# Kernel optimization log

Measured on AMD Instinct MI355X. Metric: run time of the kernel, lower is better.

Reference implementation:

```python
import jax, jax.numpy as jnp
import numpy as np

N_NODES = 100000
N_REL = 8
N_EDGES = 100000  # per relation
DIM = 128


def setup_inputs() -> dict:
    key = jax.random.key(0)
    ks = jax.random.split(key, 8)
    s = 1.0 / np.sqrt(DIM)
    return {
        "entity_embeddings": jax.random.normal(ks[0], (N_NODES, DIM), jnp.float32),
        "edge_index": jax.random.randint(ks[1], (N_REL, 2, N_EDGES), 0, N_NODES, jnp.int32),
        "edge_weights": jax.random.uniform(ks[2], (N_REL, N_EDGES), jnp.float32),
        "relW1": jax.random.normal(ks[3], (N_REL, DIM, DIM), jnp.float32) * s,
        "selfW1": jax.random.normal(ks[4], (DIM, DIM), jnp.float32) * s,
        "bias1": jnp.zeros((N_REL, DIM), jnp.float32),
        "relW2": jax.random.normal(ks[5], (N_REL, DIM, DIM), jnp.float32) * s,
        "selfW2": jax.random.normal(ks[6], (DIM, DIM), jnp.float32) * s,
        "bias2": jnp.zeros((N_REL, DIM), jnp.float32),
    }


def _wrgcn_layer(x, edge_index, edge_weights, relW, selfW, bias):
    # x: [N, Din]; edge_index: [R, 2, E]; edge_weights: [R, E]
    N = x.shape[0]
    R, _, E = edge_index.shape
    src = edge_index[:, 0]  # [R, E]
    tgt = edge_index[:, 1]  # [R, E]
    # gather -> per-relation matmul -> edge-weight scale
    src_emb = x[src]  # [R, E, Din]
    msg = jnp.einsum('red,rdo->reo', src_emb, relW) * edge_weights[..., None]  # [R, E, Dout]
    # scatter-add to target nodes (shared node space across relations)
    agg = jax.ops.segment_sum(msg.reshape(R * E, -1), tgt.reshape(R * E), num_segments=N)
    # bias added once per (relation, unique target node)
    tgt_mask = jnp.zeros((R, N), x.dtype).at[jnp.arange(R)[:, None], tgt].set(1.0)  # [R, N]
    agg = agg + jnp.einsum('rn,ro->no', tgt_mask, bias)
    # self loop
    return agg + x @ selfW


def reference(entity_embeddings, edge_index, edge_weights,
              relW1, selfW1, bias1, relW2, selfW2, bias2):
    h = _wrgcn_layer(entity_embeddings, edge_index, edge_weights, relW1, selfW1, bias1)
    h = jax.nn.relu(h)  # dropout is identity in eval mode
    out = _wrgcn_layer(h, edge_index, edge_weights, relW2, selfW2, bias2)
    return out
```

## Files before the change

kernel.cpp:

```cpp
#include <hip/hip_runtime.h>
#include <hip/hip_bf16.h>

#define NN 100000
#define DD 128
#define RR 8
#define EE 100000
#define NP1 (NN + 1)
#define NB1 98
#define PADN (NB1 * 1024)
#define SEG 8
#define WPR (NN / SEG)

typedef __attribute__((ext_vector_type(8))) short short8;
typedef __attribute__((ext_vector_type(4))) float f32x4;

__device__ __forceinline__ unsigned short f2bf(float v) {
  union { float f; unsigned int u; } x; x.f = v;
  unsigned int r = (x.u + 0x7FFFu + ((x.u >> 16) & 1u)) >> 16;
  return (unsigned short)r;
}

__global__ void k_cast4(const float* __restrict__ src, unsigned short* __restrict__ dst, int n4) {
  int i = blockIdx.x * blockDim.x + threadIdx.x;
  int stride = gridDim.x * blockDim.x;
  for (; i < n4; i += stride) {
    float4 v = reinterpret_cast<const float4*>(src)[i];
    ushort4 o;
    o.x = f2bf(v.x); o.y = f2bf(v.y); o.z = f2bf(v.z); o.w = f2bf(v.w);
    reinterpret_cast<ushort4*>(dst)[i] = o;
  }
}

__global__ void k_castT2(const float* __restrict__ s1, unsigned short* __restrict__ d1,
                         const float* __restrict__ s2, unsigned short* __restrict__ d2,
                         int total) {
  int i = blockIdx.x * blockDim.x + threadIdx.x;
  if (i >= total) return;
  const float* src = blockIdx.y ? s2 : s1;
  unsigned short* dst = blockIdx.y ? d2 : d1;
  int r = i >> 14;
  int k = (i >> 7) & 127;
  int o = i & 127;
  dst[(r << 14) + (o << 7) + k] = f2bf(src[i]);
}

__global__ void k_zero2(unsigned int* __restrict__ p1, int n1,
                        unsigned int* __restrict__ p2, int n2) {
  int i = blockIdx.x * blockDim.x + threadIdx.x;
  if (i < n1) p1[i] = 0u;
  else if (i - n1 < n2) p2[i - n1] = 0u;
}

__global__ void k_hist_mask(const int* __restrict__ edge_index, int* __restrict__ cnt,
                            unsigned int* __restrict__ mb) {
  int e = blockIdx.x * blockDim.x + threadIdx.x;
  int r = blockIdx.y;
  if (e >= EE) return;
  int tgt = edge_index[(size_t)r * 2 * EE + EE + e];
  atomicAdd(&cnt[r * PADN + tgt], 1);
  atomicOr(&mb[tgt], 1u << r);
}

__global__ void k_scan1(const int* __restrict__ cnt, int* __restrict__ start, int* __restrict__ bsum) {
  const int r = blockIdx.y, b = blockIdx.x, t = threadIdx.x;
  const int bin0 = b * 1024 + t * 4;
  int4 c = *reinterpret_cast<const int4*>(&cnt[r * PADN + bin0]);
  int s1 = c.x, s2 = s1 + c.y, s3 = s2 + c.z, tot = s3 + c.w;
  __shared__ int sh[256];
  sh[t] = tot;
  __syncthreads();
  for (int off = 1; off < 256; off <<= 1) {
    int v = (t >= off) ? sh[t - off] : 0;
    __syncthreads();
    sh[t] += v;
    __syncthreads();
  }
  int excl = sh[t] - tot;
  if (t == 255) bsum[r * NB1 + b] = sh[255];
  const int base = r * NP1;
  if (bin0 < NN) start[base + bin0] = excl;
  if (bin0 + 1 < NN) start[base + bin0 + 1] = excl + s1;
  if (bin0 + 2 < NN) start[base + bin0 + 2] = excl + s2;
  if (bin0 + 3 < NN) start[base + bin0 + 3] = excl + s3;
}

__global__ void k_scan2(const int* __restrict__ bsum, int* __restrict__ boff, int* __restrict__ start) {
  const int r = blockIdx.x, t = threadIdx.x;
  int v = (t < NB1) ? bsum[r * NB1 + t] : 0;
  __shared__ int sh[128];
  sh[t] = v;
  __syncthreads();
  for (int off = 1; off < 128; off <<= 1) {
    int u = (t >= off) ? sh[t - off] : 0;
    __syncthreads();
    sh[t] += u;
    __syncthreads();
  }
  if (t < NB1) boff[r * NB1 + t] = sh[t] - v;
  if (t == 0) start[r * NP1 + NN] = EE;
}

__global__ void k_scan3(int* __restrict__ start, const int* __restrict__ boff, int* __restrict__ cursor) {
  const int r = blockIdx.y, b = blockIdx.x, t = threadIdx.x;
  const int bin0 = b * 1024 + t * 4;
  const int off = boff[r * NB1 + b];
  const int base = r * NP1;
#pragma unroll
  for (int k = 0; k < 4; ++k) {
    int bin = bin0 + k;
    if (bin < NN) {
      int v = start[base + bin] + off;
      start[base + bin] = v;
      cursor[r * NN + bin] = v;
    }
  }
}

__global__ void k_scatter2(const int* __restrict__ edge_index, const float* __restrict__ ew,
                           int* __restrict__ cursor, int2* __restrict__ es) {
  int e = blockIdx.x * blockDim.x + threadIdx.x;
  int r = blockIdx.y;
  if (e >= EE) return;
  const int* src_p = edge_index + (size_t)r * 2 * EE;
  int tgt = src_p[EE + e];
  int pos = atomicAdd(&cursor[r * NN + tgt], 1);
  es[(size_t)r * EE + pos] = make_int2(src_p[e], __float_as_int(ew[(size_t)r * EE + e]));
}

__device__ __forceinline__ void preagg_wave(const unsigned short* __restrict__ Xsrc,
                                            const int2* __restrict__ es,
                                            const int* __restrict__ start,
                                            int r, int n0, int lane,
                                            float (&a0)[SEG], float (&a1)[SEG]) {
  const size_t rEE = (size_t)r * EE;
  int b = start[r * NP1 + n0 + (lane < 8 ? lane : 8)];
  int p[SEG + 1];
#pragma unroll
  for (int i = 0; i <= SEG; ++i) p[i] = __builtin_amdgcn_readlane(b, i);
#pragma unroll
  for (int i = 0; i < SEG; ++i) { a0[i] = 0.f; a1[i] = 0.f; }
  const int p0 = p[0];
  const int count = p[SEG] - p0;
  if (count <= 0) return;
  int rounds = 0;
#pragma unroll
  for (int i = 0; i < SEG; ++i) rounds = max(rounds, p[i + 1] - p[i]);
  const unsigned int* Xu = reinterpret_cast<const unsigned int*>(Xsrc);

  if (count <= 64) {
    int wl = lane < count ? lane : count - 1;
    int2 ew = es[rEE + p0 + wl];
    int esrc = ew.x;
    int ewbits = ew.y;
    for (int j = 0; j < rounds; ++j) {
#pragma unroll
      for (int i = 0; i < SEG; ++i) {
        int pos = p[i] + j;
        if (pos < p[i + 1]) {
          int widx = pos - p0;
          int s = __builtin_amdgcn_readlane(esrc, widx);
          float wv = __int_as_float(__builtin_amdgcn_readlane(ewbits, widx));
          unsigned int d = Xu[(size_t)s * 64 + lane];
          union { unsigned int u; float f; } lo, hi;
          lo.u = d << 16;
          hi.u = d & 0xFFFF0000u;
          a0[i] += wv * lo.f;
          a1[i] += wv * hi.f;
        }
      }
    }
  } else {
    for (int j = 0; j < rounds; ++j) {
#pragma unroll
      for (int i = 0; i < SEG; ++i) {
        int pos = p[i] + j;
        if (pos < p[i + 1]) {
          int2 e = es[rEE + pos];
          float wv = __int_as_float(e.y);
          unsigned int d = Xu[(size_t)e.x * 64 + lane];
          union { unsigned int u; float f; } lo, hi;
          lo.u = d << 16;
          hi.u = d & 0xFFFF0000u;
          a0[i] += wv * lo.f;
          a1[i] += wv * hi.f;
        }
      }
    }
  }
}

__launch_bounds__(256, 4)
__global__ void k_preagg_seg3(const unsigned short* __restrict__ Xsrc,
                              const int2* __restrict__ es, const int* __restrict__ start,
                              unsigned short* __restrict__ P0, unsigned short* __restrict__ P1,
                              unsigned short* __restrict__ P2,
                              int rbase, int nrel) {
  const int wid = blockIdx.x * 4 + (threadIdx.x >> 6);
  if (wid >= nrel * WPR) return;
  const int lane = threadIdx.x & 63;
  const int rr = wid / WPR;
  const int n0 = (wid - rr * WPR) * SEG;
  float a0[SEG], a1[SEG];
  preagg_wave(Xsrc, es, start, rbase + rr, n0, lane, a0, a1);
  unsigned short* P = (rr == 0) ? P0 : ((rr == 1) ? P1 : P2);
  unsigned int* Pw = reinterpret_cast<unsigned int*>(P);
#pragma unroll
  for (int i = 0; i < SEG; ++i)
    Pw[(size_t)(n0 + i) * 64 + lane] = (unsigned int)f2bf(a0[i]) | ((unsigned int)f2bf(a1[i]) << 16);
}

__launch_bounds__(256, 4)
__global__ void k_preagg_seg8(const unsigned short* __restrict__ Xsrc,
                              const int2* __restrict__ es, const int* __restrict__ start,
                              unsigned short* __restrict__ P0, unsigned short* __restrict__ Pws) {
  const int wid = blockIdx.x * 4 + (threadIdx.x >> 6);
  if (wid >= RR * WPR) return;
  const int lane = threadIdx.x & 63;
  const int rr = wid / WPR;
  const int n0 = (wid - rr * WPR) * SEG;
  float a0[SEG], a1[SEG];
  preagg_wave(Xsrc, es, start, rr, n0, lane, a0, a1);
  unsigned short* P = (rr == 0) ? P0 : (Pws + (size_t)(rr - 1) * NN * DD);
  unsigned int* Pw = reinterpret_cast<unsigned int*>(P);
#pragma unroll
  for (int i = 0; i < SEG; ++i)
    Pw[(size_t)(n0 + i) * 64 + lane] = (unsigned int)f2bf(a0[i]) | ((unsigned int)f2bf(a1[i]) << 16);
}

typedef const __attribute__((address_space(1))) void* gas1_t;
typedef __attribute__((address_space(3))) void* las3_t;

__device__ __forceinline__ void gl16(const void* g, void* s) {
  __builtin_amdgcn_global_load_lds((gas1_t)g, (las3_t)s, 16, 0, 0);
}

template <bool CLAMP>
__device__ __forceinline__ void stage_half(const unsigned short* __restrict__ g,
                                           unsigned short* lds, int t, int row0, int half) {
  const int w = t >> 6, l = t & 63;
  const int sub = l >> 3;
  const int sl = l & 7;
#pragma unroll
  for (int c = 0; c < 4; ++c) {
    int rb8 = c * 32 + w * 8;
    int row = rb8 + sub;
    int grow = row0 + row;
    int sr = CLAMP ? (grow < NN ? grow : NN - 1) : grow;
    const unsigned short* src = g + (size_t)sr * 128 + half * 64 + ((sl ^ (row & 7)) << 3);
    gl16(src, lds + rb8 * 64);
  }
}

__device__ __forceinline__ void mfma_half(const unsigned short* __restrict__ lA,
                                          const unsigned short* __restrict__ lB,
                                          f32x4 (&acc)[2][8], int w, int l) {
  const int lrow = l & 15, kgrp = l >> 4;
#pragma unroll
  for (int ks = 0; ks < 2; ++ks) {
    int kc = ks * 4 + kgrp;
    int ra = w * 32 + lrow;
    int rb = ra + 16;
    short8 a0 = *reinterpret_cast<const short8*>(&lA[(ra << 6) + ((kc ^ (ra & 7)) << 3)]);
    short8 a1 = *reinterpret_cast<const short8*>(&lA[(rb << 6) + ((kc ^ (rb & 7)) << 3)]);
#pragma unroll
    for (int ct = 0; ct < 8; ++ct) {
      int ro = ct * 16 + lrow;
      short8 b = *reinterpret_cast<const short8*>(&lB[(ro << 6) + ((kc ^ (ro & 7)) << 3)]);
      acc[0][ct] = __builtin_amdgcn_mfma_f32_16x16x32_bf16(a0, b, acc[0][ct], 0, 0, 0);
      acc[1][ct] = __builtin_amdgcn_mfma_f32_16x16x32_bf16(a1, b, acc[1][ct], 0, 0, 0);
    }
  }
}

template <bool CLAMP>
__device__ __forceinline__ void stage_lds(const unsigned short* __restrict__ g,
                                          unsigned short* lds, int t, int row0) {
  const int w = t >> 6, l = t & 63;
  const int sub = l >> 4, s = l & 15;
#pragma unroll
  for (int c = 0; c < 8; ++c) {
    int rowblk = c * 16 + w * 4;
    int row = rowblk + sub;
    int grow = row0 + row;
    int sr = CLAMP ? (grow < NN ? grow : NN - 1) : grow;
    const unsigned short* src = g + (size_t)sr * 128 + ((s ^ (row & 7)) << 3);
    gl16(src, lds + rowblk * 128);
  }
}

__device__ __forceinline__ void mfma_tile(const unsigned short* __restrict__ lA,
                                          const unsigned short* __restrict__ lB,
                                          f32x4 (&acc)[2][8], int w, int l) {
  const int lrow = l & 15, kgrp = l >> 4;
#pragma unroll
  for (int ks = 0; ks < 4; ++ks) {
    int kc = ks * 4 + kgrp;
    int ra = w * 32 + lrow;
    int rb = ra + 16;
    short8 a0 = *reinterpret_cast<const short8*>(&lA[(ra << 7) + ((kc ^ (ra & 7)) << 3)]);
    short8 a1 = *reinterpret_cast<const short8*>(&lA[(rb << 7) + ((kc ^ (rb & 7)) << 3)]);
#pragma unroll
    for (int ct = 0; ct < 8; ++ct) {
      int ro = ct * 16 + lrow;
      short8 b = *reinterpret_cast<const short8*>(&lB[(ro << 7) + ((kc ^ (ro & 7)) << 3)]);
      acc[0][ct] = __builtin_amdgcn_mfma_f32_16x16x32_bf16(a0, b, acc[0][ct], 0, 0, 0);
      acc[1][ct] = __builtin_amdgcn_mfma_f32_16x16x32_bf16(a1, b, acc[1][ct], 0, 0, 0);
    }
  }
}

template <bool L1>
__launch_bounds__(256, 2)
__global__ void k_gemm_fused(const unsigned short* __restrict__ Aself,
                             const unsigned short* __restrict__ Wself,
                             const unsigned short* __restrict__ P0,
                             const unsigned short* __restrict__ Pws,
                             const unsigned short* __restrict__ Wrel,
                             const unsigned int* __restrict__ maskbits,
                             const float* __restrict__ bias,
                             void* __restrict__ outp) {
  __shared__ __align__(16) unsigned short lA[2][128 * 64];
  __shared__ __align__(16) unsigned short lB[2][128 * 64];
  const int t = threadIdx.x;
  const int row0 = blockIdx.x * 128;
  const int w = t >> 6, l = t & 63;
  const int lrow = l & 15, kgrp = l >> 4;
  f32x4 acc[2][8] = {};

  auto A_of = [&](int term) -> const unsigned short* {
    return term == 0 ? Aself : (term == 1 ? P0 : Pws + (size_t)(term - 2) * NN * DD);
  };
  auto B_of = [&](int term) -> const unsigned short* {
    return term == 0 ? Wself : Wrel + ((term - 1) << 14);
  };

  stage_half<true>(A_of(0), lA[0], t, row0, 0);
  stage_half<false>(B_of(0), lB[0], t, 0, 0);
  __syncthreads();

  int cur = 0;
#pragma unroll 1
  for (int st = 0; st < 18; ++st) {
    if (st < 17) {
      int nt = (st + 1) >> 1, nh = (st + 1) & 1;
      stage_half<true>(A_of(nt), lA[cur ^ 1], t, row0, nh);
      stage_half<false>(B_of(nt), lB[cur ^ 1], t, 0, nh);
    }
    mfma_half(lA[cur], lB[cur], acc, w, l);
    __syncthreads();
    cur ^= 1;
  }

  {
    short8 a0 = {}, a1 = {}, bf[8];
#pragma unroll
    for (int ct = 0; ct < 8; ++ct) bf[ct] = short8{};
    if (kgrp == 0) {
      int ra = row0 + w * 32 + lrow;
      int rb = ra + 16;
      unsigned int ma = (ra < NN) ? maskbits[ra] : 0u;
      unsigned int mb = (rb < NN) ? maskbits[rb] : 0u;
#pragma unroll
      for (int k = 0; k < 8; ++k) {
        a0[k] = (short)(((ma >> k) & 1u) ? 0x3F80 : 0);
        a1[k] = (short)(((mb >> k) & 1u) ? 0x3F80 : 0);
      }
#pragma unroll
      for (int ct = 0; ct < 8; ++ct) {
        int o = ct * 16 + lrow;
#pragma unroll
        for (int k = 0; k < 8; ++k) bf[ct][k] = (short)f2bf(bias[k * 128 + o]);
      }
    }
#pragma unroll
    for (int ct = 0; ct < 8; ++ct) {
      acc[0][ct] = __builtin_amdgcn_mfma_f32_16x16x32_bf16(a0, bf[ct], acc[0][ct], 0, 0, 0);
      acc[1][ct] = __builtin_amdgcn_mfma_f32_16x16x32_bf16(a1, bf[ct], acc[1][ct], 0, 0, 0);
    }
  }

#pragma unroll
  for (int rt = 0; rt < 2; ++rt) {
#pragma unroll
    for (int j = 0; j < 4; ++j) {
      int grow = row0 + w * 32 + rt * 16 + kgrp * 4 + j;
      if (grow < NN) {
        if (L1) {
          unsigned short* op = (unsigned short*)outp + (size_t)grow * 128 + lrow;
#pragma unroll
          for (int ct = 0; ct < 8; ++ct) op[ct * 16] = f2bf(fmaxf(acc[rt][ct][j], 0.f));
        } else {
          float* op = (float*)outp + (size_t)grow * 128 + lrow;
#pragma unroll
          for (int ct = 0; ct < 8; ++ct) op[ct * 16] = acc[rt][ct][j];
        }
      }
    }
  }
}

template <int NT>
__launch_bounds__(256, 2)
__global__ void k_gemm_multi(const unsigned short* __restrict__ A0, const unsigned short* __restrict__ W0,
                             const unsigned short* __restrict__ A1, const unsigned short* __restrict__ W1,
                             const unsigned short* __restrict__ A2, const unsigned short* __restrict__ W2,
                             const unsigned short* __restrict__ A3, const unsigned short* __restrict__ W3,
                             float* __restrict__ outp, int accum) {
  __shared__ __align__(16) unsigned short lA[128 * 128];
  __shared__ __align__(16) unsigned short lB[128 * 128];
  const int t = threadIdx.x;
  const int row0 = blockIdx.x * 128;
  const int w = t >> 6, l = t & 63;
  const int lrow = l & 15, kgrp = l >> 4;
  f32x4 acc[2][8] = {};

  const unsigned short* As[4] = {A0, A1, A2, A3};
  const unsigned short* Ws[4] = {W0, W1, W2, W3};
#pragma unroll
  for (int term = 0; term < NT; ++term) {
    if (term) __syncthreads();
    stage_lds<true>(As[term], lA, t, row0);
    stage_lds<false>(Ws[term], lB, t, 0);
    __syncthreads();
    mfma_tile(lA, lB, acc, w, l);
  }

#pragma unroll
  for (int rt = 0; rt < 2; ++rt) {
#pragma unroll
    for (int j = 0; j < 4; ++j) {
      int grow = row0 + w * 32 + rt * 16 + kgrp * 4 + j;
      if (grow < NN) {
        float* op = outp + (size_t)grow * 128 + lrow;
        if (accum) {
#pragma unroll
          for (int ct = 0; ct < 8; ++ct) op[ct * 16] += acc[rt][ct][j];
        } else {
#pragma unroll
          for (int ct = 0; ct < 8; ++ct) op[ct * 16] = acc[rt][ct][j];
        }
      }
    }
  }
}

__global__ void k_epi1(const float* __restrict__ h32, const unsigned int* __restrict__ maskbits,
                       const float* __restrict__ bias, unsigned short* __restrict__ hb) {
  int gid = blockIdx.x * blockDim.x + threadIdx.x;
  if (gid >= NN * 32) return;
  int n = gid >> 5, c = (gid & 31) << 2;
  float4 v = *reinterpret_cast<const float4*>(h32 + (size_t)n * 128 + c);
  unsigned int mb = maskbits[n];
  float b0 = 0, b1 = 0, b2 = 0, b3 = 0;
#pragma unroll
  for (int r = 0; r < RR; ++r) {
    if ((mb >> r) & 1u) {
      const float* bp = bias + r * 128 + c;
      b0 += bp[0]; b1 += bp[1]; b2 += bp[2]; b3 += bp[3];
    }
  }
  ushort4 o;
  o.x = f2bf(fmaxf(v.x + b0, 0.f));
  o.y = f2bf(fmaxf(v.y + b1, 0.f));
  o.z = f2bf(fmaxf(v.z + b2, 0.f));
  o.w = f2bf(fmaxf(v.w + b3, 0.f));
  *reinterpret_cast<ushort4*>(hb + (size_t)n * 128 + c) = o;
}

__global__ void k_epi2(float* __restrict__ out, const unsigned int* __restrict__ maskbits,
                       const float* __restrict__ bias) {
  int gid = blockIdx.x * blockDim.x + threadIdx.x;
  if (gid >= NN * 32) return;
  int n = gid >> 5, c = (gid & 31) << 2;
  unsigned int mb = maskbits[n];
  if (!mb) return;
  float b0 = 0, b1 = 0, b2 = 0, b3 = 0;
#pragma unroll
  for (int r = 0; r < RR; ++r) {
    if ((mb >> r) & 1u) {
      const float* bp = bias + r * 128 + c;
      b0 += bp[0]; b1 += bp[1]; b2 += bp[2]; b3 += bp[3];
    }
  }
  float* p = out + (size_t)n * 128 + c;
  float4 v = *reinterpret_cast<const float4*>(p);
  v.x += b0; v.y += b1; v.z += b2; v.w += b3;
  *reinterpret_cast<float4*>(p) = v;
}

extern "C" void kernel_launch(void* const* d_in, const int* in_sizes, int n_in,
                              void* d_out, int out_size, void* d_ws, size_t ws_size,
                              hipStream_t stream) {
  const float* X   = (const float*)d_in[0];
  const int*   EI  = (const int*)d_in[1];
  const float* EW  = (const float*)d_in[2];
  const float* rW1 = (const float*)d_in[3];
  const float* sW1 = (const float*)d_in[4];
  const float* b1  = (const float*)d_in[5];
  const float* rW2 = (const float*)d_in[6];
  const float* sW2 = (const float*)d_in[7];
  const float* b2  = (const float*)d_in[8];
  float* out = (float*)d_out;
  char* ws = (char*)d_ws;

  size_t off = 0;
  auto take = [&](size_t sz) { char* p = ws + off; off += (sz + 255) & ~(size_t)255; return p; };
  unsigned short* Xb   = (unsigned short*)take((size_t)NN * DD * 2);
  unsigned short* hb   = (unsigned short*)take((size_t)NN * DD * 2);
  unsigned int*  maskb = (unsigned int*)take((size_t)NN * 4);
  unsigned short* rW1t = (unsigned short*)take((size_t)RR * DD * DD * 2);
  unsigned short* sW1t = (unsigned short*)take((size_t)DD * DD * 2);
  unsigned short* rW2t = (unsigned short*)take((size_t)RR * DD * DD * 2);
  unsigned short* sW2t = (unsigned short*)take((size_t)DD * DD * 2);
  int*   cnt    = (int*)take((size_t)RR * PADN * 4);
  int*   start  = (int*)take((size_t)RR * NP1 * 4);
  int*   cursor = (int*)take((size_t)RR * NN * 4);
  int*   bsum   = (int*)take((size_t)RR * NB1 * 4);
  int*   boff   = (int*)take((size_t)RR * NB1 * 4);
  int2*  es     = (int2*)take((size_t)RR * EE * 8);

  const size_t szReg = ((size_t)NN * DD * 2 + 255) & ~(size_t)255;
  const bool bigA = (off + 7 * szReg <= ws_size);
  unsigned short* Pws = nullptr;
  float* h32 = nullptr;
  if (bigA) {
    Pws = (unsigned short*)take(7 * szReg);
  } else {
    h32 = (float*)take((size_t)NN * DD * 4);
  }

  k_cast4<<<2048, 256, 0, stream>>>(X, Xb, NN * DD / 4);
  k_castT2<<<dim3((RR * DD * DD + 255) / 256, 2), 256, 0, stream>>>(rW1, rW1t, rW2, rW2t, RR * DD * DD);
  k_castT2<<<dim3((DD * DD + 255) / 256, 2), 256, 0, stream>>>(sW1, sW1t, sW2, sW2t, DD * DD);

  k_zero2<<<(NN + RR * PADN + 255) / 256, 256, 0, stream>>>(maskb, NN, (unsigned int*)cnt, RR * PADN);
  k_hist_mask<<<dim3((EE + 255) / 256, RR), 256, 0, stream>>>(EI, cnt, maskb);
  k_scan1<<<dim3(NB1, RR), 256, 0, stream>>>(cnt, start, bsum);
  k_scan2<<<RR, 128, 0, stream>>>(bsum, boff, start);
  k_scan3<<<dim3(NB1, RR), 256, 0, stream>>>(start, boff, cursor);
  k_scatter2<<<dim3((EE + 255) / 256, RR), 256, 0, stream>>>(EI, EW, cursor, es);

  const int nblk = (NN + 127) / 128;
  unsigned short* outu = (unsigned short*)d_out;

  if (bigA) {
    const int pblk = (RR * WPR + 3) / 4;
    k_preagg_seg8<<<pblk, 256, 0, stream>>>(Xb, es, start, outu, Pws);
    k_gemm_fused<true><<<nblk, 256, 0, stream>>>(Xb, sW1t, outu, Pws, rW1t, maskb, b1, hb);
    k_preagg_seg8<<<pblk, 256, 0, stream>>>(hb, es, start, Xb, Pws);
    k_gemm_fused<false><<<nblk, 256, 0, stream>>>(hb, sW2t, Xb, Pws, rW2t, maskb, b2, out);
  } else {
    unsigned short* h32u = (unsigned short*)h32;
    const int pblk3 = (3 * WPR + 3) / 4;
    const int pblk2 = (2 * WPR + 3) / 4;
    {
      unsigned short* P0 = outu;
      unsigned short* P1 = outu + (size_t)NN * DD;
      unsigned short* P2 = hb;
      k_preagg_seg3<<<pblk3, 256, 0, stream>>>(Xb, es, start, P0, P1, P2, 0, 3);
      k_gemm_multi<4><<<nblk, 256, 0, stream>>>(Xb, sW1t, P0, rW1t, P1, rW1t + (1 << 14), P2, rW1t + (2 << 14), h32, 0);
      k_preagg_seg3<<<pblk3, 256, 0, stream>>>(Xb, es, start, P0, P1, P2, 3, 3);
      k_gemm_multi<3><<<nblk, 256, 0, stream>>>(P0, rW1t + (3 << 14), P1, rW1t + (4 << 14), P2, rW1t + (5 << 14), nullptr, nullptr, h32, 1);
      k_preagg_seg3<<<pblk2, 256, 0, stream>>>(Xb, es, start, P0, P1, P2, 6, 2);
      k_gemm_multi<2><<<nblk, 256, 0, stream>>>(P0, rW1t + (6 << 14), P1, rW1t + (7 << 14), nullptr, nullptr, nullptr, nullptr, h32, 1);
    }
    k_epi1<<<(NN * 32 + 255) / 256, 256, 0, stream>>>(h32, maskb, b1, hb);
    {
      unsigned short* P0 = h32u;
      unsigned short* P1 = h32u + (size_t)NN * DD;
      unsigned short* P2 = Xb;
      k_preagg_seg3<<<pblk3, 256, 0, stream>>>(hb, es, start, P0, P1, P2, 0, 3);
      k_gemm_multi<4><<<nblk, 256, 0, stream>>>(hb, sW2t, P0, rW2t, P1, rW2t + (1 << 14), P2, rW2t + (2 << 14), out, 0);
      k_preagg_seg3<<<pblk3, 256, 0, stream>>>(hb, es, start, P0, P1, P2, 3, 3);
      k_gemm_multi<3><<<nblk, 256, 0, stream>>>(P0, rW2t + (3 << 14), P1, rW2t + (4 << 14), P2, rW2t + (5 << 14), nullptr, nullptr, out, 1);
      k_preagg_seg3<<<pblk2, 256, 0, stream>>>(hb, es, start, P0, P1, P2, 6, 2);
      k_gemm_multi<2><<<nblk, 256, 0, stream>>>(P0, rW2t + (6 << 14), P1, rW2t + (7 << 14), nullptr, nullptr, nullptr, nullptr, out, 1);
    }
    k_epi2<<<(NN * 32 + 255) / 256, 256, 0, stream>>>(out, maskb, b2);
  }
}
```

Baseline: 426.9 us.

## Merge prep kernels, widen preagg segments, single-buffer GEMM LDS for occupancy

Merges the weight transpose-cast and zeroing kernels into a single prep launch. Doubles the number of nodes each preagg wave handles (SEG 8 to 16) and raises the launch-bounds occupancy hints on the preagg and GEMM kernels. Turns the fused GEMM's double-buffered LDS staging into a single buffer with an extra barrier, halving shared memory so more blocks can be resident. This gives up load/compute overlap in the GEMM and may raise register pressure in preagg, since SEG 16 doubles the accumulator arrays under a tighter register cap.

```diff
diff --git a/kernel.cpp b/kernel.cpp
--- a/kernel.cpp
+++ b/kernel.cpp
@@ -8,7 +8,7 @@
 #define NP1 (NN + 1)
 #define NB1 98
 #define PADN (NB1 * 1024)
-#define SEG 8
+#define SEG 16
 #define WPR (NN / SEG)
 
 typedef __attribute__((ext_vector_type(8))) short short8;
@@ -31,25 +31,43 @@
   }
 }
 
-__global__ void k_castT2(const float* __restrict__ s1, unsigned short* __restrict__ d1,
-                         const float* __restrict__ s2, unsigned short* __restrict__ d2,
-                         int total) {
-  int i = blockIdx.x * blockDim.x + threadIdx.x;
-  if (i >= total) return;
-  const float* src = blockIdx.y ? s2 : s1;
-  unsigned short* dst = blockIdx.y ? d2 : d1;
-  int r = i >> 14;
-  int k = (i >> 7) & 127;
-  int o = i & 127;
-  dst[(r << 14) + (o << 7) + k] = f2bf(src[i]);
-}
-
-__global__ void k_zero2(unsigned int* __restrict__ p1, int n1,
-                        unsigned int* __restrict__ p2, int n2) {
-  int i = blockIdx.x * blockDim.x + threadIdx.x;
-  if (i < n1) p1[i] = 0u;
-  else if (i - n1 < n2) p2[i - n1] = 0u;
-}
+#define NWR (RR * DD * DD)
+#define NWS (DD * DD)
+__global__ void k_prep_small(const float* __restrict__ rW1, unsigned short* __restrict__ rW1t,
+                             const float* __restrict__ sW1, unsigned short* __restrict__ sW1t,
+                             const float* __restrict__ rW2, unsigned short* __restrict__ rW2t,
+                             const float* __restrict__ sW2, unsigned short* __restrict__ sW2t,
+                             unsigned int* __restrict__ maskb, unsigned int* __restrict__ cnt) {
+  int j = blockIdx.x * blockDim.x + threadIdx.x;
+  if (j < NWR) {
+    int r = j >> 14, k = (j >> 7) & 127, o = j & 127;
+    rW1t[(r << 14) + (o << 7) + k] = f2bf(rW1[j]);
+    return;
+  }
+  j -= NWR;
+  if (j < NWR) {
+    int r = j >> 14, k = (j >> 7) & 127, o = j & 127;
+    rW2t[(r << 14) + (o << 7) + k] = f2bf(rW2[j]);
+    return;
+  }
+  j -= NWR;
+  if (j < NWS) {
+    int k = j >> 7, o = j & 127;
+    sW1t[(o << 7) + k] = f2bf(sW1[j]);
+    return;
+  }
+  j -= NWS;
+  if (j < NWS) {
+    int k = j >> 7, o = j & 127;
+    sW2t[(o << 7) + k] = f2bf(sW2[j]);
+    return;
+  }
+  j -= NWS;
+  if (j < NN) { maskb[j] = 0u; return; }
+  j -= NN;
+  if (j < RR * PADN) cnt[j] = 0u;
+}
+#define PREP_TOTAL (2 * NWR + 2 * NWS + NN + RR * PADN)
 
 __global__ void k_hist_mask(const int* __restrict__ edge_index, int* __restrict__ cnt,
                             unsigned int* __restrict__ mb) {
@@ -133,7 +151,7 @@
                                             int r, int n0, int lane,
                                             float (&a0)[SEG], float (&a1)[SEG]) {
   const size_t rEE = (size_t)r * EE;
-  int b = start[r * NP1 + n0 + (lane < 8 ? lane : 8)];
+  int b = start[r * NP1 + n0 + (lane < SEG ? lane : SEG)];
   int p[SEG + 1];
 #pragma unroll
   for (int i = 0; i <= SEG; ++i) p[i] = __builtin_amdgcn_readlane(b, i);
@@ -189,7 +207,7 @@
   }
 }
 
-__launch_bounds__(256, 4)
+__launch_bounds__(256, 8)
 __global__ void k_preagg_seg3(const unsigned short* __restrict__ Xsrc,
                               const int2* __restrict__ es, const int* __restrict__ start,
                               unsigned short* __restrict__ P0, unsigned short* __restrict__ P1,
@@ -209,7 +227,7 @@
     Pw[(size_t)(n0 + i) * 64 + lane] = (unsigned int)f2bf(a0[i]) | ((unsigned int)f2bf(a1[i]) << 16);
 }
 
-__launch_bounds__(256, 4)
+__launch_bounds__(256, 8)
 __global__ void k_preagg_seg8(const unsigned short* __restrict__ Xsrc,
                               const int2* __restrict__ es, const int* __restrict__ start,
                               unsigned short* __restrict__ P0, unsigned short* __restrict__ Pws) {
@@ -310,7 +328,7 @@
 }
 
 template <bool L1>
-__launch_bounds__(256, 2)
+__launch_bounds__(256, 4)
 __global__ void k_gemm_fused(const unsigned short* __restrict__ Aself,
                              const unsigned short* __restrict__ Wself,
                              const unsigned short* __restrict__ P0,
@@ -319,8 +337,8 @@
                              const unsigned int* __restrict__ maskbits,
                              const float* __restrict__ bias,
                              void* __restrict__ outp) {
-  __shared__ __align__(16) unsigned short lA[2][128 * 64];
-  __shared__ __align__(16) unsigned short lB[2][128 * 64];
+  __shared__ __align__(16) unsigned short lA[128 * 64];
+  __shared__ __align__(16) unsigned short lB[128 * 64];
   const int t = threadIdx.x;
   const int row0 = blockIdx.x * 128;
   const int w = t >> 6, l = t & 63;
@@ -334,21 +352,14 @@
     return term == 0 ? Wself : Wrel + ((term - 1) << 14);
   };
 
-  stage_half<true>(A_of(0), lA[0], t, row0, 0);
-  stage_half<false>(B_of(0), lB[0], t, 0, 0);
-  __syncthreads();
-
-  int cur = 0;
 #pragma unroll 1
   for (int st = 0; st < 18; ++st) {
-    if (st < 17) {
-      int nt = (st + 1) >> 1, nh = (st + 1) & 1;
-      stage_half<true>(A_of(nt), lA[cur ^ 1], t, row0, nh);
-      stage_half<false>(B_of(nt), lB[cur ^ 1], t, 0, nh);
-    }
-    mfma_half(lA[cur], lB[cur], acc, w, l);
+    int nt = st >> 1, nh = st & 1;
+    stage_half<true>(A_of(nt), lA, t, row0, nh);
+    stage_half<false>(B_of(nt), lB, t, 0, nh);
     __syncthreads();
-    cur ^= 1;
+    mfma_half(lA, lB, acc, w, l);
+    if (st < 17) __syncthreads();
   }
 
   {
@@ -530,10 +541,10 @@
   }
 
   k_cast4<<<2048, 256, 0, stream>>>(X, Xb, NN * DD / 4);
-  k_castT2<<<dim3((RR * DD * DD + 255) / 256, 2), 256, 0, stream>>>(rW1, rW1t, rW2, rW2t, RR * DD * DD);
-  k_castT2<<<dim3((DD * DD + 255) / 256, 2), 256, 0, stream>>>(sW1, sW1t, sW2, sW2t, DD * DD);
-
-  k_zero2<<<(NN + RR * PADN + 255) / 256, 256, 0, stream>>>(maskb, NN, (unsigned int*)cnt, RR * PADN);
+  k_prep_small<<<(PREP_TOTAL + 255) / 256, 256, 0, stream>>>(rW1, rW1t, sW1, sW1t,
+                                                             rW2, rW2t, sW2, sW2t,
+                                                             maskb, (unsigned int*)cnt);
+
   k_hist_mask<<<dim3((EE + 255) / 256, RR), 256, 0, stream>>>(EI, cnt, maskb);
   k_scan1<<<dim3(NB1, RR), 256, 0, stream>>>(cnt, start, bsum);
   k_scan2<<<RR, 128, 0, stream>>>(bsum, boff, start);
```

New measurement: 434.9 us. No clear change (+1.9%).
